# Kernel optimization log

Measured on AMD Instinct MI355X. Metric: run time of the kernel, lower is better.

## Reference

```python
import jax, jax.numpy as jnp
import numpy as np

NUM_HEADS = 16
NUM_KV_HEADS = 4
HEAD_DIM = 128
HIDDEN = 2048
SEQ = 2048
BATCH = 2
Q_PER_GROUP = NUM_HEADS // NUM_KV_HEADS          # 4
GROUP_SIZE = (Q_PER_GROUP + 2) * HEAD_DIM        # 768
TOTAL_PROJ = NUM_KV_HEADS * GROUP_SIZE           # 3072


def setup_inputs() -> dict:
    key = jax.random.key(0)
    k1, k2, k3 = jax.random.split(key, 3)
    x = jax.random.normal(k1, (SEQ, BATCH, HIDDEN), dtype=jnp.float32)
    w_qkv = jax.random.normal(k2, (TOTAL_PROJ, HIDDEN), dtype=jnp.float32) * 0.02
    w_proj = jax.random.normal(k3, (HIDDEN, NUM_HEADS * HEAD_DIM), dtype=jnp.float32) * 0.02
    return {"x": x, "w_qkv": w_qkv, "w_proj": w_proj}


def reference(x, w_qkv, w_proj):
    s, b, _ = x.shape
    # fused QKV projection (GQA-packed layout: per kv-group [q...q, k, v])
    qkv = jnp.einsum('sbh,ph->sbp', x, w_qkv)                       # [s,b,3072]
    qkv = qkv.reshape(s, b, NUM_KV_HEADS, GROUP_SIZE)
    q = qkv[..., :Q_PER_GROUP * HEAD_DIM].reshape(s, b, NUM_HEADS, HEAD_DIM)
    k = qkv[..., Q_PER_GROUP * HEAD_DIM:(Q_PER_GROUP + 1) * HEAD_DIM]  # [s,b,kvh,d]
    v = qkv[..., (Q_PER_GROUP + 1) * HEAD_DIM:]                        # [s,b,kvh,d]
    # to [b, heads, s, d]; expand kv heads over query groups (GQA)
    q = q.transpose(1, 2, 0, 3)
    k = jnp.repeat(k.transpose(1, 2, 0, 3), Q_PER_GROUP, axis=1)
    v = jnp.repeat(v.transpose(1, 2, 0, 3), Q_PER_GROUP, axis=1)
    scale = 1.0 / jnp.sqrt(jnp.asarray(HEAD_DIM, dtype=x.dtype))
    scores = jnp.einsum('bhsd,bhtd->bhst', q, k) * scale           # [b,h,s,s]
    attn = jax.nn.softmax(scores, axis=-1)
    out = jnp.einsum('bhst,bhtd->bhsd', attn, v)                    # [b,h,s,d]
    out = out.transpose(2, 0, 1, 3).reshape(s, b, NUM_HEADS * HEAD_DIM)
    return jnp.einsum('sbe,he->sbh', out, w_proj)                   # [s,b,hidden]
```

## Files before the change

### kernel.cpp

```cpp
#include <hip/hip_runtime.h>
#include <hip/hip_bf16.h>

typedef __bf16 bf16;
typedef __bf16 bf16x8 __attribute__((ext_vector_type(8)));
typedef __bf16 bf16x4v __attribute__((ext_vector_type(4)));
typedef float  f32x4  __attribute__((ext_vector_type(4)));
typedef float  f32x16 __attribute__((ext_vector_type(16)));

#define SEQL  2048
#define BATCH 2
#define HID   2048
#define NH    16
#define NKVH  4
#define HD    128
#define NPROJ 3072
#define MROWS 4096

#define QSCALE (0.08838834764831845f * 1.44269504088896340f)

__device__ __forceinline__ void gload16(const void* src, void* dst) {
  __builtin_amdgcn_global_load_lds(
      (__attribute__((address_space(1))) void*)src,
      (__attribute__((address_space(3))) void*)dst, 16, 0, 0);
}

__device__ __forceinline__ int swz128(int off) { return off ^ (((off >> 7) & 7) << 4); }
__device__ __forceinline__ int swz256(int off) { return off ^ (((off >> 8) & 7) << 4); }

__device__ __forceinline__ unsigned cvtpk_bf16(float lo, float hi) {
  unsigned r;
  asm("v_cvt_pk_bf16_f32 %0, %1, %2" : "=v"(r) : "v"(lo), "v"(hi));
  return r;
}
__device__ __forceinline__ void permswap32(unsigned& a, unsigned& b) {
  asm volatile("v_permlane32_swap_b32 %0, %1" : "+v"(a), "+v"(b));
}
__device__ __forceinline__ f32x16 mfma16(bf16x8 a, bf16x8 b, f32x16 c) {
  return __builtin_amdgcn_mfma_f32_32x32x16_bf16(a, b, c, 0, 0, 0);
}

__global__ __launch_bounds__(256) void cvt_kernel(
    const float* __restrict__ x, const float* __restrict__ wq, const float* __restrict__ wp,
    bf16* __restrict__ xo, bf16* __restrict__ wqo, bf16* __restrict__ wpo) {
  const int NXQ  = (MROWS * HID) / 4;
  const int NWQQ = (NPROJ * HID) / 4;
  const int NWPQ = (HID * HID) / 4;
  const int total = NXQ + NWQQ + NWPQ;
  for (int i = blockIdx.x * blockDim.x + threadIdx.x; i < total; i += gridDim.x * blockDim.x) {
    const float4* src; bf16* dst; int j;
    if (i < NXQ)            { src = (const float4*)x;  dst = xo;  j = i; }
    else if (i < NXQ + NWQQ){ src = (const float4*)wq; dst = wqo; j = i - NXQ; }
    else                    { src = (const float4*)wp; dst = wpo; j = i - NXQ - NWQQ; }
    float4 v = src[j];
    bf16x4v o;
    o[0] = (bf16)v.x; o[1] = (bf16)v.y; o[2] = (bf16)v.z; o[3] = (bf16)v.w;
    *(bf16x4v*)(dst + (size_t)j * 4) = o;
  }
}

__global__ __launch_bounds__(256, 3) void qkv_gemm(
    const bf16* __restrict__ A, const bf16* __restrict__ B,
    bf16* __restrict__ Qo, bf16* __restrict__ Ko, bf16* __restrict__ Vt) {
  __shared__ char lds[32768];
  const int tid = threadIdx.x, l = tid & 63, w = tid >> 6;
  const int lin = blockIdx.x + 24 * blockIdx.y;
  const int swz = (lin & 7) * 96 + (lin >> 3);
  const int bx = swz % 24, by = swz / 24;
  const int r0 = by * 128, p0 = bx * 128;
  const int wr = w >> 1, wc = w & 1;

  f32x4 acc[4][4];
  const f32x4 fzero = {0.f, 0.f, 0.f, 0.f};
#pragma unroll
  for (int m = 0; m < 4; m++)
#pragma unroll
    for (int n = 0; n < 4; n++) acc[m][n] = fzero;

  for (int kt = 0; kt < HID / 64; ++kt) {
    const int k0 = kt * 64;
    __syncthreads();
#pragma unroll
    for (int q = 0; q < 4; q++) {
      const int doff = (w * 4 + q) * 1024 + l * 16;
      const int row = doff >> 7;
      const int chv = ((doff >> 4) & 7) ^ (row & 7);
      gload16((const char*)A + ((size_t)(r0 + row) * HID + k0) * 2 + chv * 16,
              lds + (w * 4 + q) * 1024);
      gload16((const char*)B + ((size_t)(p0 + row) * HID + k0) * 2 + chv * 16,
              lds + 16384 + (w * 4 + q) * 1024);
    }
    __syncthreads();
    bf16x8 af[4][2], bfr[4][2];
#pragma unroll
    for (int m = 0; m < 4; m++)
#pragma unroll
      for (int kk = 0; kk < 2; kk++) {
        int off = (wr * 64 + m * 16 + (l & 15)) * 128 + kk * 64 + (l >> 4) * 16;
        af[m][kk] = *(const bf16x8*)(lds + swz128(off));
      }
#pragma unroll
    for (int n = 0; n < 4; n++)
#pragma unroll
      for (int kk = 0; kk < 2; kk++) {
        int off = (wc * 64 + n * 16 + (l & 15)) * 128 + kk * 64 + (l >> 4) * 16;
        bfr[n][kk] = *(const bf16x8*)(lds + 16384 + swz128(off));
      }
#pragma unroll
    for (int kk = 0; kk < 2; kk++)
#pragma unroll
      for (int m = 0; m < 4; m++)
#pragma unroll
        for (int n = 0; n < 4; n++)
          acc[m][n] = __builtin_amdgcn_mfma_f32_16x16x32_bf16(af[m][kk], bfr[n][kk], acc[m][n], 0, 0, 0);
  }

  const int seg = (p0 % 768) / 128;
  const int g = p0 / 768;
#pragma unroll
  for (int m = 0; m < 4; m++) {
    const int rbase = r0 + wr * 64 + m * 16 + ((l >> 4) << 2);
#pragma unroll
    for (int n = 0; n < 4; n++) {
      const int c = wc * 64 + n * 16 + (l & 15);
#pragma unroll
      for (int rg = 0; rg < 4; ++rg) {
        const int r = rbase + rg;
        const int s = r >> 1, b = r & 1;
        if (seg < 4) {
          const int h = g * 4 + seg;
          Qo[(((size_t)(b * 16 + h)) * 2048 + s) * 128 + c] = (bf16)(acc[m][n][rg] * QSCALE);
        } else if (seg == 4) {
          Ko[(((size_t)(b * 4 + g)) * 2048 + s) * 128 + c] = (bf16)acc[m][n][rg];
        } else {
          Vt[(((size_t)(b * 4 + g)) * 128 + c) * 2048 + s] = (bf16)acc[m][n][rg];
        }
      }
    }
  }
}

template<int BASE>
__device__ __forceinline__ void attn_tile(
    char* lds, const bf16x8* qf, const int* ka, const int* va,
    f32x16* oacc, f32x16& lacc, bf16x8 ones) {
  const f32x16 z16 = {};

  f32x16 sT0 = z16, sT1 = z16;
  __builtin_amdgcn_s_setprio(1);
#pragma unroll
  for (int s = 0; s < 8; s++) {
    bf16x8 kf = *(const bf16x8*)(lds + BASE + ka[s]);
    sT0 = mfma16(kf, qf[s], sT0);
  }
#pragma unroll
  for (int s = 0; s < 8; s++) {
    bf16x8 kf = *(const bf16x8*)(lds + BASE + ka[8 + s]);
    sT1 = mfma16(kf, qf[s], sT1);
  }
  __builtin_amdgcn_s_setprio(0);

  unsigned c0[8], c1[8];
#pragma unroll
  for (int i = 0; i < 16; i++) sT0[i] = exp2f(sT0[i]);
#pragma unroll
  for (int i = 0; i < 8; i++) c0[i] = cvtpk_bf16(sT0[2 * i], sT0[2 * i + 1]);
  permswap32(c0[0], c0[2]); permswap32(c0[1], c0[3]);
  permswap32(c0[4], c0[6]); permswap32(c0[5], c0[7]);

  __builtin_amdgcn_s_setprio(1);
#pragma unroll
  for (int ks = 0; ks < 2; ks++) {
    union { unsigned u[4]; bf16x8 v; } pb;
#pragma unroll
    for (int i = 0; i < 4; i++) pb.u[i] = c0[(ks & 1) * 4 + i];
    lacc = mfma16(ones, pb.v, lacc);
#pragma unroll
    for (int dblk = 0; dblk < 4; dblk++) {
      bf16x8 vf = *(const bf16x8*)(lds + BASE + 16384 + va[ks * 4 + dblk]);
      oacc[dblk] = mfma16(vf, pb.v, oacc[dblk]);
    }
  }
  __builtin_amdgcn_s_setprio(0);

#pragma unroll
  for (int i = 0; i < 16; i++) sT1[i] = exp2f(sT1[i]);
#pragma unroll
  for (int i = 0; i < 8; i++) c1[i] = cvtpk_bf16(sT1[2 * i], sT1[2 * i + 1]);
  permswap32(c1[0], c1[2]); permswap32(c1[1], c1[3]);
  permswap32(c1[4], c1[6]); permswap32(c1[5], c1[7]);

  __builtin_amdgcn_s_setprio(1);
#pragma unroll
  for (int ks = 2; ks < 4; ks++) {
    union { unsigned u[4]; bf16x8 v; } pb;
#pragma unroll
    for (int i = 0; i < 4; i++) pb.u[i] = c1[(ks & 1) * 4 + i];
    lacc = mfma16(ones, pb.v, lacc);
#pragma unroll
    for (int dblk = 0; dblk < 4; dblk++) {
      bf16x8 vf = *(const bf16x8*)(lds + BASE + 16384 + va[ks * 4 + dblk]);
      oacc[dblk] = mfma16(vf, pb.v, oacc[dblk]);
    }
  }
  __builtin_amdgcn_s_setprio(0);
}

__global__ __launch_bounds__(256, 2) void attn_kernel(
    const bf16* __restrict__ Q, const bf16* __restrict__ K, const bf16* __restrict__ V,
    bf16* __restrict__ O) {
  __shared__ char lds[65536];
  const int tid = threadIdx.x, l = tid & 63, w = tid >> 6;
  const int l31 = l & 31, h2 = l >> 5;
  const int lin = blockIdx.x + (blockIdx.y << 4);
  const int swzb = (lin & 7) * 64 + (lin >> 3);
  const int qt = swzb & 15, bh = swzb >> 4;
  const int b = bh >> 4, head = bh & 15, g = head >> 2;

  const int q0 = qt * 128 + w * 32;

  bf16x8 qf[8];
  {
    const bf16* qbase = Q + (((size_t)(b * 16 + head)) * 2048 + q0 + l31) * 128 + h2 * 8;
#pragma unroll
    for (int s = 0; s < 8; s++) qf[s] = *(const bf16x8*)(qbase + s * 16);
  }

  int ka[16], va[16];
#pragma unroll
  for (int tsub = 0; tsub < 2; tsub++)
#pragma unroll
    for (int s = 0; s < 8; s++)
      ka[tsub * 8 + s] = swz256((tsub * 32 + l31) * 256 + s * 32 + h2 * 16);
#pragma unroll
  for (int ks = 0; ks < 4; ks++)
#pragma unroll
    for (int dblk = 0; dblk < 4; dblk++)
      va[ks * 4 + dblk] = swz128((dblk * 32 + l31) * 128 + ks * 32 + h2 * 16);

  int kso[4], vso[4];
#pragma unroll
  for (int q = 0; q < 4; q++) {
    const int off = (q * 4 + w) * 1024 + l * 16;
    kso[q] = swz256(off);
    const int rowv = off >> 7;
    const int chv = ((off >> 4) & 7) ^ (rowv & 7);
    vso[q] = rowv * 4096 + chv * 16;
  }

  bf16x8 ones;
#pragma unroll
  for (int i = 0; i < 8; i++) ones[i] = (bf16)1.0f;

  const f32x16 z16 = {};
  f32x16 oacc[4];
#pragma unroll
  for (int d = 0; d < 4; d++) oacc[d] = z16;
  f32x16 lacc = z16;

  const char* kbase = (const char*)(K + ((size_t)(b * 4 + g)) * 2048 * 128);
  const char* vbase = (const char*)(V + ((size_t)(b * 4 + g)) * 128 * 2048);

  auto stage = [&](int t0, int B) {
#pragma unroll
    for (int q = 0; q < 4; q++) {
      gload16(kbase + (size_t)t0 * 256 + kso[q], lds + B + (q * 4 + w) * 1024);
      gload16(vbase + (size_t)t0 * 2 + vso[q], lds + B + 16384 + (q * 4 + w) * 1024);
    }
  };

  stage(0, 0);
  __syncthreads();

  for (int t0 = 0; t0 < SEQL; t0 += 128) {
    stage(t0 + 64, 32768);
    attn_tile<0>(lds, qf, ka, va, oacc, lacc, ones);
    __syncthreads();
    if (t0 + 128 < SEQL) stage(t0 + 128, 0);
    attn_tile<32768>(lds, qf, ka, va, oacc, lacc, ones);
    __syncthreads();
  }

  const float inv = 1.0f / lacc[0];
  const size_t rowo = ((size_t)(q0 + l31) * 2 + b) * 2048 + (size_t)head * 128;
#pragma unroll
  for (int dblk = 0; dblk < 4; dblk++)
#pragma unroll
    for (int g4 = 0; g4 < 4; g4++) {
      bf16x4v ov;
#pragma unroll
      for (int e = 0; e < 4; e++) ov[e] = (bf16)(oacc[dblk][g4 * 4 + e] * inv);
      *(bf16x4v*)(O + rowo + dblk * 32 + g4 * 8 + h2 * 4) = ov;
    }
}

__global__ __launch_bounds__(256, 2) void proj_gemm(
    const bf16* __restrict__ A, const bf16* __restrict__ B, float* __restrict__ C) {
  __shared__ char lds[32768];
  const int tid = threadIdx.x, l = tid & 63, w = tid >> 6;
  const int lin = blockIdx.x + (blockIdx.y << 4);
  const int swz = (lin & 7) * 64 + (lin >> 3);
  const int bx = swz & 15, by = swz >> 4;
  const int r0 = by * 128, p0 = bx * 128;
  const int wr = w >> 1, wc = w & 1;

  f32x4 acc[4][4];
  const f32x4 fzero = {0.f, 0.f, 0.f, 0.f};
#pragma unroll
  for (int m = 0; m < 4; m++)
#pragma unroll
    for (int n = 0; n < 4; n++) acc[m][n] = fzero;

  for (int kt = 0; kt < HID / 64; ++kt) {
    const int k0 = kt * 64;
    __syncthreads();
#pragma unroll
    for (int q = 0; q < 4; q++) {
      const int doff = (w * 4 + q) * 1024 + l * 16;
      const int row = doff >> 7;
      const int chv = ((doff >> 4) & 7) ^ (row & 7);
      gload16((const char*)A + ((size_t)(r0 + row) * HID + k0) * 2 + chv * 16,
              lds + (w * 4 + q) * 1024);
      gload16((const char*)B + ((size_t)(p0 + row) * HID + k0) * 2 + chv * 16,
              lds + 16384 + (w * 4 + q) * 1024);
    }
    __syncthreads();
    bf16x8 af[4][2], bfr[4][2];
#pragma unroll
    for (int m = 0; m < 4; m++)
#pragma unroll
      for (int kk = 0; kk < 2; kk++) {
        int off = (wr * 64 + m * 16 + (l & 15)) * 128 + kk * 64 + (l >> 4) * 16;
        af[m][kk] = *(const bf16x8*)(lds + swz128(off));
      }
#pragma unroll
    for (int n = 0; n < 4; n++)
#pragma unroll
      for (int kk = 0; kk < 2; kk++) {
        int off = (wc * 64 + n * 16 + (l & 15)) * 128 + kk * 64 + (l >> 4) * 16;
        bfr[n][kk] = *(const bf16x8*)(lds + 16384 + swz128(off));
      }
#pragma unroll
    for (int kk = 0; kk < 2; kk++)
#pragma unroll
      for (int m = 0; m < 4; m++)
#pragma unroll
        for (int n = 0; n < 4; n++)
          acc[m][n] = __builtin_amdgcn_mfma_f32_16x16x32_bf16(af[m][kk], bfr[n][kk], acc[m][n], 0, 0, 0);
  }
#pragma unroll
  for (int m = 0; m < 4; m++) {
    const int rbase = r0 + wr * 64 + m * 16 + ((l >> 4) << 2);
#pragma unroll
    for (int n = 0; n < 4; n++) {
      const int c = p0 + wc * 64 + n * 16 + (l & 15);
#pragma unroll
      for (int rg = 0; rg < 4; ++rg)
        C[(size_t)(rbase + rg) * HID + c] = acc[m][n][rg];
    }
  }
}

extern "C" void kernel_launch(void* const* d_in, const int* in_sizes, int n_in,
                              void* d_out, int out_size, void* d_ws, size_t ws_size,
                              hipStream_t stream) {
  const float* x  = (const float*)d_in[0];
  const float* wq = (const float*)d_in[1];
  const float* wp = (const float*)d_in[2];
  float* out = (float*)d_out;
  char* ws = (char*)d_ws;

  size_t off = 0;
  bf16* xb  = (bf16*)(ws + off); off += (size_t)MROWS * HID * 2;
  bf16* wqb = (bf16*)(ws + off); off += (size_t)NPROJ * HID * 2;
  bf16* wpb = (bf16*)(ws + off); off += (size_t)HID * HID * 2;
  bf16* Qb  = (bf16*)(ws + off); off += (size_t)2 * 16 * 2048 * 128 * 2;
  bf16* Kb  = (bf16*)(ws + off); off += (size_t)2 * 4 * 2048 * 128 * 2;
  bf16* Vb  = (bf16*)(ws + off); off += (size_t)2 * 4 * 128 * 2048 * 2;
  bf16* Ob  = xb;

  cvt_kernel<<<2048, 256, 0, stream>>>(x, wq, wp, xb, wqb, wpb);
  qkv_gemm<<<dim3(24, 32), 256, 0, stream>>>(xb, wqb, Qb, Kb, Vb);
  attn_kernel<<<dim3(16, 32), 256, 0, stream>>>(Qb, Kb, Vb, Ob);
  proj_gemm<<<dim3(16, 32), 256, 0, stream>>>(Ob, wpb, out);
}
```

Baseline: 204.8 us.

## Single-buffer V tiles in LDS to fit three attention blocks per CU

The attention kernel keeps double buffering for K but uses a single LDS buffer for V. This shrinks shared memory from 64KB to 48KB, and the launch bounds are raised to allow three blocks per CU. Each V load is now issued just before a barrier, so its latency is exposed, and each loop iteration gains two extra barriers. The aim is for the extra resident waves to hide that latency. The tighter register budget under three blocks per CU may also force spills.

```diff
diff --git a/kernel.cpp b/kernel.cpp
--- a/kernel.cpp
+++ b/kernel.cpp
@@ -139,7 +139,7 @@
   }
 }
 
-template<int BASE>
+template<int KBASE>
 __device__ __forceinline__ void attn_tile(
     char* lds, const bf16x8* qf, const int* ka, const int* va,
     f32x16* oacc, f32x16& lacc, bf16x8 ones) {
@@ -149,12 +149,12 @@
   __builtin_amdgcn_s_setprio(1);
 #pragma unroll
   for (int s = 0; s < 8; s++) {
-    bf16x8 kf = *(const bf16x8*)(lds + BASE + ka[s]);
+    bf16x8 kf = *(const bf16x8*)(lds + KBASE + ka[s]);
     sT0 = mfma16(kf, qf[s], sT0);
   }
 #pragma unroll
   for (int s = 0; s < 8; s++) {
-    bf16x8 kf = *(const bf16x8*)(lds + BASE + ka[8 + s]);
+    bf16x8 kf = *(const bf16x8*)(lds + KBASE + ka[8 + s]);
     sT1 = mfma16(kf, qf[s], sT1);
   }
   __builtin_amdgcn_s_setprio(0);
@@ -176,7 +176,7 @@
     lacc = mfma16(ones, pb.v, lacc);
 #pragma unroll
     for (int dblk = 0; dblk < 4; dblk++) {
-      bf16x8 vf = *(const bf16x8*)(lds + BASE + 16384 + va[ks * 4 + dblk]);
+      bf16x8 vf = *(const bf16x8*)(lds + 32768 + va[ks * 4 + dblk]);
       oacc[dblk] = mfma16(vf, pb.v, oacc[dblk]);
     }
   }
@@ -198,17 +198,17 @@
     lacc = mfma16(ones, pb.v, lacc);
 #pragma unroll
     for (int dblk = 0; dblk < 4; dblk++) {
-      bf16x8 vf = *(const bf16x8*)(lds + BASE + 16384 + va[ks * 4 + dblk]);
+      bf16x8 vf = *(const bf16x8*)(lds + 32768 + va[ks * 4 + dblk]);
       oacc[dblk] = mfma16(vf, pb.v, oacc[dblk]);
     }
   }
   __builtin_amdgcn_s_setprio(0);
 }
 
-__global__ __launch_bounds__(256, 2) void attn_kernel(
+__global__ __launch_bounds__(256, 3) void attn_kernel(
     const bf16* __restrict__ Q, const bf16* __restrict__ K, const bf16* __restrict__ V,
     bf16* __restrict__ O) {
-  __shared__ char lds[65536];
+  __shared__ char lds[49152];
   const int tid = threadIdx.x, l = tid & 63, w = tid >> 6;
   const int l31 = l & 31, h2 = l >> 5;
   const int lin = blockIdx.x + (blockIdx.y << 4);
@@ -260,23 +260,31 @@
   const char* kbase = (const char*)(K + ((size_t)(b * 4 + g)) * 2048 * 128);
   const char* vbase = (const char*)(V + ((size_t)(b * 4 + g)) * 128 * 2048);
 
-  auto stage = [&](int t0, int B) {
-#pragma unroll
-    for (int q = 0; q < 4; q++) {
+  auto stageK = [&](int t0, int B) {
+#pragma unroll
+    for (int q = 0; q < 4; q++)
       gload16(kbase + (size_t)t0 * 256 + kso[q], lds + B + (q * 4 + w) * 1024);
-      gload16(vbase + (size_t)t0 * 2 + vso[q], lds + B + 16384 + (q * 4 + w) * 1024);
-    }
   };
-
-  stage(0, 0);
+  auto stageV = [&](int t0) {
+#pragma unroll
+    for (int q = 0; q < 4; q++)
+      gload16(vbase + (size_t)t0 * 2 + vso[q], lds + 32768 + (q * 4 + w) * 1024);
+  };
+
+  stageK(0, 0);
+  stageV(0);
   __syncthreads();
 
   for (int t0 = 0; t0 < SEQL; t0 += 128) {
-    stage(t0 + 64, 32768);
+    stageK(t0 + 64, 16384);
     attn_tile<0>(lds, qf, ka, va, oacc, lacc, ones);
     __syncthreads();
-    if (t0 + 128 < SEQL) stage(t0 + 128, 0);
-    attn_tile<32768>(lds, qf, ka, va, oacc, lacc, ones);
+    stageV(t0 + 64);
+    __syncthreads();
+    if (t0 + 128 < SEQL) stageK(t0 + 128, 0);
+    attn_tile<16384>(lds, qf, ka, va, oacc, lacc, ones);
+    __syncthreads();
+    if (t0 + 128 < SEQL) stageV(t0 + 128);
     __syncthreads();
   }
 
```

Measured after the change: 671.8 us. 3.28x slower.

## Fuse w_proj conversion into attention kernel and compute softmax row sum with VALU

Applied to the files above, without the earlier changes.

Conversion of w_proj from fp32 to bf16 moves out of the standalone cvt kernel and into the prologue of the attention kernel, where each block converts a slice. This shortens the bandwidth-bound conversion pass and hides that work behind the compute-bound attention. The softmax denominator is now a per-lane VALU sum of the exponentials, combined across half-waves with a shuffle at the end, in place of the extra MFMA against a vector of ones. That removes four MFMAs per tile but adds VALU adds, and the denominator is summed in fp32 rather than from bf16-rounded probabilities.

```diff
diff --git a/kernel.cpp b/kernel.cpp
--- a/kernel.cpp
+++ b/kernel.cpp
@@ -38,19 +38,24 @@
 __device__ __forceinline__ f32x16 mfma16(bf16x8 a, bf16x8 b, f32x16 c) {
   return __builtin_amdgcn_mfma_f32_32x32x16_bf16(a, b, c, 0, 0, 0);
 }
+__device__ __forceinline__ float sum16(const f32x16& v) {
+  float a = (v[0] + v[1]) + (v[2] + v[3]);
+  float b = (v[4] + v[5]) + (v[6] + v[7]);
+  float c = (v[8] + v[9]) + (v[10] + v[11]);
+  float d = (v[12] + v[13]) + (v[14] + v[15]);
+  return (a + b) + (c + d);
+}
 
 __global__ __launch_bounds__(256) void cvt_kernel(
-    const float* __restrict__ x, const float* __restrict__ wq, const float* __restrict__ wp,
-    bf16* __restrict__ xo, bf16* __restrict__ wqo, bf16* __restrict__ wpo) {
+    const float* __restrict__ x, const float* __restrict__ wq,
+    bf16* __restrict__ xo, bf16* __restrict__ wqo) {
   const int NXQ  = (MROWS * HID) / 4;
   const int NWQQ = (NPROJ * HID) / 4;
-  const int NWPQ = (HID * HID) / 4;
-  const int total = NXQ + NWQQ + NWPQ;
+  const int total = NXQ + NWQQ;
   for (int i = blockIdx.x * blockDim.x + threadIdx.x; i < total; i += gridDim.x * blockDim.x) {
     const float4* src; bf16* dst; int j;
-    if (i < NXQ)            { src = (const float4*)x;  dst = xo;  j = i; }
-    else if (i < NXQ + NWQQ){ src = (const float4*)wq; dst = wqo; j = i - NXQ; }
-    else                    { src = (const float4*)wp; dst = wpo; j = i - NXQ - NWQQ; }
+    if (i < NXQ) { src = (const float4*)x;  dst = xo;  j = i; }
+    else         { src = (const float4*)wq; dst = wqo; j = i - NXQ; }
     float4 v = src[j];
     bf16x4v o;
     o[0] = (bf16)v.x; o[1] = (bf16)v.y; o[2] = (bf16)v.z; o[3] = (bf16)v.w;
@@ -142,7 +147,7 @@
 template<int BASE>
 __device__ __forceinline__ void attn_tile(
     char* lds, const bf16x8* qf, const int* ka, const int* va,
-    f32x16* oacc, f32x16& lacc, bf16x8 ones) {
+    f32x16* oacc, float& lp) {
   const f32x16 z16 = {};
 
   f32x16 sT0 = z16, sT1 = z16;
@@ -162,6 +167,7 @@
   unsigned c0[8], c1[8];
 #pragma unroll
   for (int i = 0; i < 16; i++) sT0[i] = exp2f(sT0[i]);
+  lp += sum16(sT0);
 #pragma unroll
   for (int i = 0; i < 8; i++) c0[i] = cvtpk_bf16(sT0[2 * i], sT0[2 * i + 1]);
   permswap32(c0[0], c0[2]); permswap32(c0[1], c0[3]);
@@ -173,7 +179,6 @@
     union { unsigned u[4]; bf16x8 v; } pb;
 #pragma unroll
     for (int i = 0; i < 4; i++) pb.u[i] = c0[(ks & 1) * 4 + i];
-    lacc = mfma16(ones, pb.v, lacc);
 #pragma unroll
     for (int dblk = 0; dblk < 4; dblk++) {
       bf16x8 vf = *(const bf16x8*)(lds + BASE + 16384 + va[ks * 4 + dblk]);
@@ -184,6 +189,7 @@
 
 #pragma unroll
   for (int i = 0; i < 16; i++) sT1[i] = exp2f(sT1[i]);
+  lp += sum16(sT1);
 #pragma unroll
   for (int i = 0; i < 8; i++) c1[i] = cvtpk_bf16(sT1[2 * i], sT1[2 * i + 1]);
   permswap32(c1[0], c1[2]); permswap32(c1[1], c1[3]);
@@ -195,7 +201,6 @@
     union { unsigned u[4]; bf16x8 v; } pb;
 #pragma unroll
     for (int i = 0; i < 4; i++) pb.u[i] = c1[(ks & 1) * 4 + i];
-    lacc = mfma16(ones, pb.v, lacc);
 #pragma unroll
     for (int dblk = 0; dblk < 4; dblk++) {
       bf16x8 vf = *(const bf16x8*)(lds + BASE + 16384 + va[ks * 4 + dblk]);
@@ -207,10 +212,24 @@
 
 __global__ __launch_bounds__(256, 2) void attn_kernel(
     const bf16* __restrict__ Q, const bf16* __restrict__ K, const bf16* __restrict__ V,
-    bf16* __restrict__ O) {
+    bf16* __restrict__ O, const float* __restrict__ wp, bf16* __restrict__ wpb) {
   __shared__ char lds[65536];
   const int tid = threadIdx.x, l = tid & 63, w = tid >> 6;
   const int l31 = l & 31, h2 = l >> 5;
+
+  {
+    const int bid = blockIdx.x + (blockIdx.y << 4);
+    const int base = bid * 256 + tid;
+#pragma unroll
+    for (int k = 0; k < 8; k++) {
+      const int i = base + k * 131072;
+      float4 v = ((const float4*)wp)[i];
+      bf16x4v o;
+      o[0] = (bf16)v.x; o[1] = (bf16)v.y; o[2] = (bf16)v.z; o[3] = (bf16)v.w;
+      *(bf16x4v*)(wpb + (size_t)i * 4) = o;
+    }
+  }
+
   const int lin = blockIdx.x + (blockIdx.y << 4);
   const int swzb = (lin & 7) * 64 + (lin >> 3);
   const int qt = swzb & 15, bh = swzb >> 4;
@@ -247,15 +266,11 @@
     vso[q] = rowv * 4096 + chv * 16;
   }
 
-  bf16x8 ones;
-#pragma unroll
-  for (int i = 0; i < 8; i++) ones[i] = (bf16)1.0f;
-
   const f32x16 z16 = {};
   f32x16 oacc[4];
 #pragma unroll
   for (int d = 0; d < 4; d++) oacc[d] = z16;
-  f32x16 lacc = z16;
+  float lp = 0.f;
 
   const char* kbase = (const char*)(K + ((size_t)(b * 4 + g)) * 2048 * 128);
   const char* vbase = (const char*)(V + ((size_t)(b * 4 + g)) * 128 * 2048);
@@ -273,14 +288,14 @@
 
   for (int t0 = 0; t0 < SEQL; t0 += 128) {
     stage(t0 + 64, 32768);
-    attn_tile<0>(lds, qf, ka, va, oacc, lacc, ones);
+    attn_tile<0>(lds, qf, ka, va, oacc, lp);
     __syncthreads();
     if (t0 + 128 < SEQL) stage(t0 + 128, 0);
-    attn_tile<32768>(lds, qf, ka, va, oacc, lacc, ones);
-    __syncthreads();
-  }
-
-  const float inv = 1.0f / lacc[0];
+    attn_tile<32768>(lds, qf, ka, va, oacc, lp);
+    __syncthreads();
+  }
+
+  const float inv = 1.0f / (lp + __shfl_xor(lp, 32));
   const size_t rowo = ((size_t)(q0 + l31) * 2 + b) * 2048 + (size_t)head * 128;
 #pragma unroll
   for (int dblk = 0; dblk < 4; dblk++)
@@ -378,8 +393,8 @@
   bf16* Vb  = (bf16*)(ws + off); off += (size_t)2 * 4 * 128 * 2048 * 2;
   bf16* Ob  = xb;
 
-  cvt_kernel<<<2048, 256, 0, stream>>>(x, wq, wp, xb, wqb, wpb);
+  cvt_kernel<<<2048, 256, 0, stream>>>(x, wq, xb, wqb);
   qkv_gemm<<<dim3(24, 32), 256, 0, stream>>>(xb, wqb, Qb, Kb, Vb);
-  attn_kernel<<<dim3(16, 32), 256, 0, stream>>>(Qb, Kb, Vb, Ob);
+  attn_kernel<<<dim3(16, 32), 256, 0, stream>>>(Qb, Kb, Vb, Ob, wp, wpb);
   proj_gemm<<<dim3(16, 32), 256, 0, stream>>>(Ob, wpb, out);
 }
```

After: 201.8 us. No clear change (-1.5%).

## Retile QKV GEMM to 256x256 double-buffered blocks and sum softmax denominators in VALU

Applied to the files above, without the earlier changes.

The QKV projection GEMM moves from 128x128 tiles with 256 threads and a single LDS buffer to 256x256 tiles with 512 threads. It uses a double-buffered 128KB LDS pipeline with explicit vmcnt waits and barriers, aiming for more operand reuse and load/compute overlap. The attention kernel drops the extra MFMA with a ones vector that accumulated the row sum. Instead each lane adds its exp values in VALU and the two half-waves are combined with a shuffle. The trade-offs are fewer GEMM blocks (192) at one block per CU and extra VALU adds in the attention inner loop.

```diff
diff --git a/kernel.cpp b/kernel.cpp
--- a/kernel.cpp
+++ b/kernel.cpp
@@ -37,6 +37,13 @@
 }
 __device__ __forceinline__ f32x16 mfma16(bf16x8 a, bf16x8 b, f32x16 c) {
   return __builtin_amdgcn_mfma_f32_32x32x16_bf16(a, b, c, 0, 0, 0);
+}
+__device__ __forceinline__ float sum16(const f32x16& v) {
+  float a = (v[0] + v[1]) + (v[2] + v[3]);
+  float b = (v[4] + v[5]) + (v[6] + v[7]);
+  float c = (v[8] + v[9]) + (v[10] + v[11]);
+  float d = (v[12] + v[13]) + (v[14] + v[15]);
+  return (a + b) + (c + d);
 }
 
 __global__ __launch_bounds__(256) void cvt_kernel(
@@ -58,70 +65,106 @@
   }
 }
 
-__global__ __launch_bounds__(256, 3) void qkv_gemm(
+__global__ __launch_bounds__(512) void qkv_gemm(
     const bf16* __restrict__ A, const bf16* __restrict__ B,
     bf16* __restrict__ Qo, bf16* __restrict__ Ko, bf16* __restrict__ Vt) {
-  __shared__ char lds[32768];
+  __shared__ char lds[131072];
   const int tid = threadIdx.x, l = tid & 63, w = tid >> 6;
-  const int lin = blockIdx.x + 24 * blockIdx.y;
-  const int swz = (lin & 7) * 96 + (lin >> 3);
-  const int bx = swz % 24, by = swz / 24;
-  const int r0 = by * 128, p0 = bx * 128;
-  const int wr = w >> 1, wc = w & 1;
-
-  f32x4 acc[4][4];
+  const int wm = w >> 2, wn = w & 3;
+  const int lin = blockIdx.x;
+  const int swz = (lin & 7) * 24 + (lin >> 3);
+  const int bx = swz % 12, by = swz / 12;
+  const int r0 = by * 256, p0 = bx * 256;
+
+  f32x4 acc[8][4];
   const f32x4 fzero = {0.f, 0.f, 0.f, 0.f};
 #pragma unroll
-  for (int m = 0; m < 4; m++)
+  for (int m = 0; m < 8; m++)
 #pragma unroll
     for (int n = 0; n < 4; n++) acc[m][n] = fzero;
 
-  for (int kt = 0; kt < HID / 64; ++kt) {
-    const int k0 = kt * 64;
-    __syncthreads();
+  int sr[4], sc[4];
+#pragma unroll
+  for (int q = 0; q < 4; q++) {
+    const int doff = (q * 512 + tid) * 16;
+    sr[q] = doff >> 7;
+    sc[q] = ((((doff >> 4) & 7) ^ (sr[q] & 7)) << 4);
+  }
+
+  int aoff[8][2], boff[4][2];
+#pragma unroll
+  for (int m = 0; m < 8; m++)
+#pragma unroll
+    for (int kk = 0; kk < 2; kk++)
+      aoff[m][kk] = swz128((wm * 128 + m * 16 + (l & 15)) * 128 + kk * 64 + (l >> 4) * 16);
+#pragma unroll
+  for (int n = 0; n < 4; n++)
+#pragma unroll
+    for (int kk = 0; kk < 2; kk++)
+      boff[n][kk] = swz128((wn * 64 + n * 16 + (l & 15)) * 128 + kk * 64 + (l >> 4) * 16);
+
+  auto stage = [&](int t, int buf) {
+    const int k0 = t * 64;
 #pragma unroll
     for (int q = 0; q < 4; q++) {
-      const int doff = (w * 4 + q) * 1024 + l * 16;
-      const int row = doff >> 7;
-      const int chv = ((doff >> 4) & 7) ^ (row & 7);
-      gload16((const char*)A + ((size_t)(r0 + row) * HID + k0) * 2 + chv * 16,
-              lds + (w * 4 + q) * 1024);
-      gload16((const char*)B + ((size_t)(p0 + row) * HID + k0) * 2 + chv * 16,
-              lds + 16384 + (w * 4 + q) * 1024);
-    }
-    __syncthreads();
-    bf16x8 af[4][2], bfr[4][2];
-#pragma unroll
-    for (int m = 0; m < 4; m++)
-#pragma unroll
-      for (int kk = 0; kk < 2; kk++) {
-        int off = (wr * 64 + m * 16 + (l & 15)) * 128 + kk * 64 + (l >> 4) * 16;
-        af[m][kk] = *(const bf16x8*)(lds + swz128(off));
-      }
-#pragma unroll
-    for (int n = 0; n < 4; n++)
-#pragma unroll
-      for (int kk = 0; kk < 2; kk++) {
-        int off = (wc * 64 + n * 16 + (l & 15)) * 128 + kk * 64 + (l >> 4) * 16;
-        bfr[n][kk] = *(const bf16x8*)(lds + 16384 + swz128(off));
-      }
-#pragma unroll
-    for (int kk = 0; kk < 2; kk++)
-#pragma unroll
-      for (int m = 0; m < 4; m++)
+      gload16((const char*)A + ((size_t)(r0 + sr[q]) * HID + k0) * 2 + sc[q],
+              lds + buf * 32768 + (q * 512 + (w * 64)) * 16);
+      gload16((const char*)B + ((size_t)(p0 + sr[q]) * HID + k0) * 2 + sc[q],
+              lds + 65536 + buf * 32768 + (q * 512 + (w * 64)) * 16);
+    }
+  };
+
+  auto compute = [&](int t) {
+    const int bufb = (t & 1) * 32768;
+#pragma unroll
+    for (int kk = 0; kk < 2; kk++) {
+      bf16x8 af[8], bfv[4];
+#pragma unroll
+      for (int m = 0; m < 8; m++)
+        af[m] = *(const bf16x8*)(lds + bufb + aoff[m][kk]);
+#pragma unroll
+      for (int n = 0; n < 4; n++)
+        bfv[n] = *(const bf16x8*)(lds + 65536 + bufb + boff[n][kk]);
+#pragma unroll
+      for (int m = 0; m < 8; m++)
 #pragma unroll
         for (int n = 0; n < 4; n++)
-          acc[m][n] = __builtin_amdgcn_mfma_f32_16x16x32_bf16(af[m][kk], bfr[n][kk], acc[m][n], 0, 0, 0);
-  }
-
-  const int seg = (p0 % 768) / 128;
-  const int g = p0 / 768;
-#pragma unroll
-  for (int m = 0; m < 4; m++) {
-    const int rbase = r0 + wr * 64 + m * 16 + ((l >> 4) << 2);
+          acc[m][n] = __builtin_amdgcn_mfma_f32_16x16x32_bf16(af[m], bfv[n], acc[m][n], 0, 0, 0);
+    }
+  };
+
+  stage(0, 0);
+  stage(1, 1);
+  asm volatile("s_waitcnt vmcnt(8)" ::: "memory");
+  __builtin_amdgcn_sched_barrier(0);
+  __builtin_amdgcn_s_barrier();
+  __builtin_amdgcn_sched_barrier(0);
+
+  for (int t = 0; t < HID / 64; ++t) {
+    compute(t);
+    __builtin_amdgcn_sched_barrier(0);
+    __builtin_amdgcn_s_barrier();
+    __builtin_amdgcn_sched_barrier(0);
+    if (t + 2 < HID / 64) {
+      stage(t + 2, t & 1);
+      asm volatile("s_waitcnt vmcnt(8)" ::: "memory");
+    } else if (t + 1 < HID / 64) {
+      asm volatile("s_waitcnt vmcnt(0)" ::: "memory");
+    }
+    __builtin_amdgcn_sched_barrier(0);
+    __builtin_amdgcn_s_barrier();
+    __builtin_amdgcn_sched_barrier(0);
+  }
+
+#pragma unroll
+  for (int m = 0; m < 8; m++) {
+    const int rbase = r0 + wm * 128 + m * 16 + ((l >> 4) << 2);
 #pragma unroll
     for (int n = 0; n < 4; n++) {
-      const int c = wc * 64 + n * 16 + (l & 15);
+      const int pc = p0 + wn * 64 + n * 16;
+      const int seg = (pc % 768) / 128;
+      const int g = pc / 768;
+      const int c = (pc % 128) + (l & 15);
 #pragma unroll
       for (int rg = 0; rg < 4; ++rg) {
         const int r = rbase + rg;
@@ -142,7 +185,7 @@
 template<int BASE>
 __device__ __forceinline__ void attn_tile(
     char* lds, const bf16x8* qf, const int* ka, const int* va,
-    f32x16* oacc, f32x16& lacc, bf16x8 ones) {
+    f32x16* oacc, float& lp) {
   const f32x16 z16 = {};
 
   f32x16 sT0 = z16, sT1 = z16;
@@ -162,6 +205,7 @@
   unsigned c0[8], c1[8];
 #pragma unroll
   for (int i = 0; i < 16; i++) sT0[i] = exp2f(sT0[i]);
+  lp += sum16(sT0);
 #pragma unroll
   for (int i = 0; i < 8; i++) c0[i] = cvtpk_bf16(sT0[2 * i], sT0[2 * i + 1]);
   permswap32(c0[0], c0[2]); permswap32(c0[1], c0[3]);
@@ -173,7 +217,6 @@
     union { unsigned u[4]; bf16x8 v; } pb;
 #pragma unroll
     for (int i = 0; i < 4; i++) pb.u[i] = c0[(ks & 1) * 4 + i];
-    lacc = mfma16(ones, pb.v, lacc);
 #pragma unroll
     for (int dblk = 0; dblk < 4; dblk++) {
       bf16x8 vf = *(const bf16x8*)(lds + BASE + 16384 + va[ks * 4 + dblk]);
@@ -184,6 +227,7 @@
 
 #pragma unroll
   for (int i = 0; i < 16; i++) sT1[i] = exp2f(sT1[i]);
+  lp += sum16(sT1);
 #pragma unroll
   for (int i = 0; i < 8; i++) c1[i] = cvtpk_bf16(sT1[2 * i], sT1[2 * i + 1]);
   permswap32(c1[0], c1[2]); permswap32(c1[1], c1[3]);
@@ -195,7 +239,6 @@
     union { unsigned u[4]; bf16x8 v; } pb;
 #pragma unroll
     for (int i = 0; i < 4; i++) pb.u[i] = c1[(ks & 1) * 4 + i];
-    lacc = mfma16(ones, pb.v, lacc);
 #pragma unroll
     for (int dblk = 0; dblk < 4; dblk++) {
       bf16x8 vf = *(const bf16x8*)(lds + BASE + 16384 + va[ks * 4 + dblk]);
@@ -247,15 +290,11 @@
     vso[q] = rowv * 4096 + chv * 16;
   }
 
-  bf16x8 ones;
-#pragma unroll
-  for (int i = 0; i < 8; i++) ones[i] = (bf16)1.0f;
-
   const f32x16 z16 = {};
   f32x16 oacc[4];
 #pragma unroll
   for (int d = 0; d < 4; d++) oacc[d] = z16;
-  f32x16 lacc = z16;
+  float lp = 0.f;
 
   const char* kbase = (const char*)(K + ((size_t)(b * 4 + g)) * 2048 * 128);
   const char* vbase = (const char*)(V + ((size_t)(b * 4 + g)) * 128 * 2048);
@@ -273,14 +312,14 @@
 
   for (int t0 = 0; t0 < SEQL; t0 += 128) {
     stage(t0 + 64, 32768);
-    attn_tile<0>(lds, qf, ka, va, oacc, lacc, ones);
+    attn_tile<0>(lds, qf, ka, va, oacc, lp);
     __syncthreads();
     if (t0 + 128 < SEQL) stage(t0 + 128, 0);
-    attn_tile<32768>(lds, qf, ka, va, oacc, lacc, ones);
+    attn_tile<32768>(lds, qf, ka, va, oacc, lp);
     __syncthreads();
   }
 
-  const float inv = 1.0f / lacc[0];
+  const float inv = 1.0f / (lp + __shfl_xor(lp, 32));
   const size_t rowo = ((size_t)(q0 + l31) * 2 + b) * 2048 + (size_t)head * 128;
 #pragma unroll
   for (int dblk = 0; dblk < 4; dblk++)
@@ -379,7 +418,7 @@
   bf16* Ob  = xb;
 
   cvt_kernel<<<2048, 256, 0, stream>>>(x, wq, wp, xb, wqb, wpb);
-  qkv_gemm<<<dim3(24, 32), 256, 0, stream>>>(xb, wqb, Qb, Kb, Vb);
+  qkv_gemm<<<dim3(192), 512, 0, stream>>>(xb, wqb, Qb, Kb, Vb);
   attn_kernel<<<dim3(16, 32), 256, 0, stream>>>(Qb, Kb, Vb, Ob);
   proj_gemm<<<dim3(16, 32), 256, 0, stream>>>(Ob, wpb, out);
 }
```

Result: slower. 210.9 us (+3.0%).
